# Kernel optimization log

Measured on AMD Instinct MI355X. Metric: run time of the kernel, lower is better.

Reference implementation:

```python
import jax, jax.numpy as jnp
import numpy as np

B, T, DM, DS = 8, 2048, 1024, 256
BASE_DECAY = 0.05


def _lin(k, out_dim, in_dim):
    return jax.random.normal(k, (out_dim, in_dim), jnp.float32) / np.sqrt(in_dim).astype(np.float32)


def setup_inputs() -> dict:
    key = jax.random.key(0)
    ks = jax.random.split(key, 18)
    return {
        "x": jax.random.normal(ks[0], (B, T, DM), jnp.float32),
        "prev_state": jax.random.normal(ks[1], (B, DS), jnp.float32),
        "W_in": _lin(ks[2], DS, DM),
        "W_x": _lin(ks[3], DS, DM),
        "W_s": _lin(ks[4], DS, DS),
        "W_out": _lin(ks[5], DM, DS),
        "W_gx": _lin(ks[6], DS, DM),
        "b_gx": jax.random.normal(ks[7], (DS,), jnp.float32) * 0.02,
        "W_gs": _lin(ks[8], DS, DS),
        "b_gs": jax.random.normal(ks[9], (DS,), jnp.float32) * 0.02,
        "W_dc": _lin(ks[10], DS, DM + DS),
        "b_dc": jax.random.normal(ks[11], (DS,), jnp.float32) * 0.02,
        "W_pp": _lin(ks[12], DS, 2 * DS),
        "b_pp": jax.random.normal(ks[13], (DS,), jnp.float32) * 0.02,
        "W_pg": _lin(ks[14], DS, DS),
        "b_pg": jax.random.normal(ks[15], (DS,), jnp.float32) * 0.02,
    }


def reference(x, prev_state, W_in, W_x, W_s, W_out, W_gx, b_gx, W_gs, b_gs,
              W_dc, b_dc, W_pp, b_pp, W_pg, b_pg):
    # torch Linear: y = x @ W.T (+ b); W is [out, in]
    lin = lambda v, W: jnp.einsum('bti,oi->bto', v, W)
    Bx, Tx, _ = x.shape
    delta = lin(x, W_in)                                   # [B,T,DS]
    s_prev = jnp.broadcast_to(prev_state[:, None, :], (Bx, Tx, prev_state.shape[-1]))
    ctx = jnp.concatenate([x, s_prev], axis=-1)            # [B,T,DM+DS]
    decay = jnp.exp(-BASE_DECAY * jnp.clip(jax.nn.sigmoid(lin(ctx, W_dc) + b_dc), 0.0, 1.0))
    s_pred = s_prev * decay + delta + lin(x, W_x) + 0.5 * lin(s_prev, W_s)
    perturb_in = jnp.concatenate([s_pred, s_prev], axis=-1)  # [B,T,2*DS]
    perturb_vec = jnp.tanh(lin(perturb_in, W_pp) + b_pp)
    perturb_strength = jax.nn.sigmoid(lin(s_prev, W_pg) + b_pg)
    s_corrected = s_pred + perturb_strength * perturb_vec
    gate_in = jax.nn.sigmoid(lin(x, W_gx) + b_gx)
    gate_state = jax.nn.sigmoid(lin(s_prev, W_gs) + b_gs)
    h = s_corrected * gate_in * gate_state
    out = lin(h, W_out)                                    # [B,T,DM]
    return out, h[:, -1, :]
```

## Files before the change

kernel.cpp:

```cpp
#include <hip/hip_runtime.h>
#include <hip/hip_bf16.h>
#include <math.h>


typedef __attribute__((ext_vector_type(4)))  float f32x4;
typedef __attribute__((ext_vector_type(8)))  short bf16x8;

#define DEV static __device__ __forceinline__

DEV float bf2f(short u) {
  union { float f; unsigned i; } v; v.i = ((unsigned)(unsigned short)u) << 16; return v.f;
}
DEV short f2bf(float f) {
  union { float f; unsigned i; } v; v.f = f;
  unsigned x = v.i;
  return (short)((x + 0x7fffu + ((x >> 16) & 1u)) >> 16);
}
DEV unsigned pk_bf16(float lo, float hi) {
  __hip_bfloat162 h = __float22bfloat162_rn(make_float2(lo, hi));
  return *(unsigned*)&h;
}
DEV float sigmoidf_(float x) { return 1.f / (1.f + expf(-x)); }

DEV void gl16(const void* g, void* l) {
  __builtin_amdgcn_global_load_lds(
      (const __attribute__((address_space(1))) void*)(g),
      (__attribute__((address_space(3))) void*)(l), 16, 0, 0);
}

static const size_t OFF_S    = 0;
static const size_t OFF_G    = 8388608;
static const size_t OFF_XBF  = 25165824;
static const size_t OFF_WCAT = OFF_XBF + 33554432;
static const size_t OFF_WPP  = OFF_WCAT + 1572864;
static const size_t OFF_WOUT = OFF_WPP + 131072;
static const size_t OFF_VEC  = OFF_WOUT + 524288;

__global__ __launch_bounds__(256, 1) void prep_all_k(
    const float* __restrict__ x, short* __restrict__ xbf,
    const float* __restrict__ W_in, const float* __restrict__ W_x,
    const float* __restrict__ W_gx, const float* __restrict__ W_dc,
    const float* __restrict__ W_pp, const float* __restrict__ W_out,
    short* __restrict__ wcat, short* __restrict__ wpp, short* __restrict__ wout,
    const float* __restrict__ prev, const float* __restrict__ Ws,
    const float* __restrict__ bdc, const float* __restrict__ bpp,
    const float* __restrict__ Wpg, const float* __restrict__ bpg,
    const float* __restrict__ Wgs, const float* __restrict__ bgs,
    float* __restrict__ vecs) {
  const int bid = (int)blockIdx.x, tid = (int)threadIdx.x;
  if (bid < 8192) {
    const size_t i = ((size_t)bid * 256 + tid) * 8;
    const float4 a = *(const float4*)(x + i);
    const float4 b = *(const float4*)(x + i + 4);
    uint4 o;
    o.x = pk_bf16(a.x, a.y); o.y = pk_bf16(a.z, a.w);
    o.z = pk_bf16(b.x, b.y); o.w = pk_bf16(b.z, b.w);
    *(uint4*)(xbf + i) = o;
  } else if (bid < 12544) {
    const int idx = (bid - 8192) * 256 + tid;
    const int N_WCAT = 768 * 1024, N_WPP = 256 * 256;
    if (idx < N_WCAT) {
      const int r = idx >> 10, k = idx & 1023;
      const int g = r / 192, j = r % 192;
      float v;
      if (j < 64)       v = W_in[(g * 64 + j) * 1024 + k] + W_x[(g * 64 + j) * 1024 + k];
      else if (j < 128) v = W_gx[(g * 64 + j - 64) * 1024 + k];
      else              v = W_dc[(g * 64 + j - 128) * 1280 + k];
      wcat[idx] = f2bf(v);
    } else if (idx < N_WCAT + N_WPP) {
      const int j = idx - N_WCAT, o = j >> 8, k = j & 255;
      wpp[j] = f2bf(W_pp[o * 512 + k]);
    } else {
      const int j = idx - N_WCAT - N_WPP, o = j >> 8, k = j & 255;
      wout[j] = f2bf(W_out[o * 256 + k]);
    }
  } else {
    const int sb = bid - 12544;
    const int b = sb / 20, rem = sb % 20, m = rem >> 2, oq = rem & 3;
    const int lane = tid & 63, w = tid >> 6;
    const float4 sv = *(const float4*)(prev + b * 256 + lane * 4);
    const float* Wb; const float* bias; int stride, off;
    if (m == 0)      { Wb = W_dc; stride = 1280; off = 1024; bias = bdc; }
    else if (m == 1) { Wb = Ws;   stride = 256;  off = 0;    bias = nullptr; }
    else if (m == 2) { Wb = W_pp; stride = 512;  off = 256;  bias = bpp; }
    else if (m == 3) { Wb = Wpg;  stride = 256;  off = 0;    bias = bpg; }
    else             { Wb = Wgs;  stride = 256;  off = 0;    bias = bgs; }
    const int o0 = oq * 64 + w * 16;
#pragma unroll 4
    for (int i = 0; i < 16; ++i) {
      const int o = o0 + i;
      const float4 wv = *(const float4*)(Wb + (size_t)o * stride + off + lane * 4);
      float p = wv.x * sv.x + wv.y * sv.y + wv.z * sv.z + wv.w * sv.w;
#pragma unroll
      for (int d = 32; d >= 1; d >>= 1) p += __shfl_xor(p, d, 64);
      if (lane == 0) {
        float r = (m == 1) ? 0.5f * p : p + bias[o];
        if (m >= 3) r = sigmoidf_(r);
        vecs[m * 2048 + b * 256 + o] = r;
      }
    }
  }
}

__global__ __launch_bounds__(512) void gemm1sg8p_k(const short* __restrict__ A,
                                                   const short* __restrict__ Bm,
                                                   const float* __restrict__ prev,
                                                   const float* __restrict__ bgx,
                                                   const float* __restrict__ vecs,
                                                   short* __restrict__ S,
                                                   short* __restrict__ G) {
  __shared__ short As[4][8192];
  __shared__ short Bs[2][12288];
  const int tid = (int)threadIdx.x, lane = tid & 63, w = tid >> 6;
  int bid = (int)blockIdx.x;
  bid = (bid & 7) * 32 + (bid >> 3);
  const int mt = bid >> 2, grp = bid & 3;
  const int m0 = mt * 256, b = m0 >> 11;
  const short* gA = A + (size_t)m0 * 1024;
  const short* gB = Bm + (size_t)(grp * 192) * 1024;

  f32x4 acc[2][12];
#pragma unroll
  for (int mi = 0; mi < 2; ++mi)
#pragma unroll
    for (int ni = 0; ni < 12; ++ni)
#pragma unroll
      for (int r = 0; r < 4; ++r) acc[mi][ni][r] = 0.f;

#define STGA(lds, half, t)                                                    \
  {                                                                           \
    _Pragma("unroll")                                                         \
    for (int j = 0; j < 2; ++j) {                                             \
      const int Gr = j * 512 + tid, r = Gr >> 3, g = Gr & 7;                  \
      gl16(gA + (size_t)((half) * 128 + r) * 1024 + (t) * 64 +                \
               ((g ^ (r & 7)) * 8),                                           \
           (lds) + Gr * 8);                                                   \
    }                                                                         \
  }
#define STGB(lds, t)                                                          \
  {                                                                           \
    _Pragma("unroll")                                                         \
    for (int j = 0; j < 3; ++j) {                                             \
      const int Gr = j * 512 + tid, r = Gr >> 3, g = Gr & 7;                  \
      gl16(gB + (size_t)r * 1024 + (t) * 64 + ((g ^ (r & 7)) * 8),            \
           (lds) + Gr * 8);                                                   \
    }                                                                         \
  }

  STGA(As[0], 0, 0); STGA(As[1], 1, 0);
  STGB(Bs[0], 0);
  STGA(As[2], 0, 1);
  asm volatile("s_waitcnt vmcnt(2)" ::: "memory");
  __builtin_amdgcn_s_barrier();

  const int arow = lane & 15, ag = lane >> 4;
  const int rA = (w & 3) * 32;
  const int hA = w >> 2;
  bf16x8 af[2][2], bfv[4][2];
#pragma unroll 1
  for (int t = 0; t < 16; ++t) {
    const short* sA = As[(2 * t + hA) & 3];
    const short* sB = Bs[t & 1];
#pragma unroll
    for (int q = 0; q < 3; ++q) {
      if (q == 0) {
#pragma unroll
        for (int mi = 0; mi < 2; ++mi) {
          const int r = rA + mi * 16 + arow;
#pragma unroll
          for (int ks = 0; ks < 2; ++ks)
            af[mi][ks] = *(const bf16x8*)(sA + r * 64 + (((ks * 4 + ag) ^ (r & 7)) << 3));
        }
      }
#pragma unroll
      for (int fj = 0; fj < 4; ++fj) {
        const int r = q * 64 + fj * 16 + arow;
#pragma unroll
        for (int ks = 0; ks < 2; ++ks)
          bfv[fj][ks] = *(const bf16x8*)(sB + r * 64 + (((ks * 4 + ag) ^ (r & 7)) << 3));
      }
      if (q == 0) {
        if (t + 1 < 16) {
          STGB(Bs[(t + 1) & 1], t + 1);
          STGA(As[(2 * t + 3) & 3], 1, t + 1);
        }
      } else if (q == 2) {
        if (t + 2 < 16) STGA(As[(2 * t + 4) & 3], 0, t + 2);
        if (t <= 13) { asm volatile("s_waitcnt vmcnt(2)" ::: "memory"); }
        else         { asm volatile("s_waitcnt vmcnt(0)" ::: "memory"); }
      }
      __builtin_amdgcn_s_barrier();
      __builtin_amdgcn_s_setprio(1);
#pragma unroll
      for (int mi = 0; mi < 2; ++mi)
#pragma unroll
        for (int fj = 0; fj < 4; ++fj)
#pragma unroll
          for (int ks = 0; ks < 2; ++ks)
            acc[mi][q * 4 + fj] = __builtin_amdgcn_mfma_f32_16x16x32_bf16(
                af[mi][ks], bfv[fj][ks], acc[mi][q * 4 + fj], 0, 0, 0);
      __builtin_amdgcn_s_setprio(0);
      __builtin_amdgcn_s_barrier();
    }
  }
#undef STGA
#undef STGB

  const int quad = lane >> 4;
#pragma unroll
  for (int cidx = 0; cidx < 4; ++cidx) {
    const int cg = grp * 64 + cidx * 16 + arow;
    const float sdc = vecs[0 * 2048 + b * 256 + cg];
    const float sws = vecs[1 * 2048 + b * 256 + cg];
    const float pv  = prev[b * 256 + cg];
    const float bg  = bgx[cg];
#pragma unroll
    for (int mi = 0; mi < 2; ++mi)
#pragma unroll
      for (int r = 0; r < 4; ++r) {
        const int row = m0 + w * 32 + mi * 16 + quad * 4 + r;
        const float dec = expf(-0.05f * sigmoidf_(acc[mi][8 + cidx][r] + sdc));
        const float sp = pv * dec + acc[mi][cidx][r] + sws;
        const float g = sigmoidf_(acc[mi][4 + cidx][r] + bg);
        S[(size_t)row * 256 + cg] = f2bf(sp);
        G[(size_t)row * 256 + cg] = f2bf(g);
      }
  }
}

__global__ __launch_bounds__(256) void gemm2h_k(const short* __restrict__ S,
                                                const short* __restrict__ G,
                                                const short* __restrict__ Wpp,
                                                const float* __restrict__ vecs,
                                                short* __restrict__ H,
                                                float* __restrict__ out) {
  __shared__ short As2[2][2048];
  __shared__ short Bs2[2][4096];
  const int tid = (int)threadIdx.x, lane = tid & 63, w = tid >> 6;
  const int wr = w >> 1, wc = w & 1;
  int bid = (int)blockIdx.x;
  bid = (bid & 7) * 64 + (bid >> 3);
  const int m0 = (bid >> 1) * 64, n0 = (bid & 1) * 128;
  const int b = m0 >> 11;
  const short* gA = S + (size_t)m0 * 256;
  const short* gB = Wpp + (size_t)n0 * 256;

  f32x4 acc[2][4];
#pragma unroll
  for (int mi = 0; mi < 2; ++mi)
#pragma unroll
    for (int ni = 0; ni < 4; ++ni)
#pragma unroll
      for (int r = 0; r < 4; ++r) acc[mi][ni][r] = 0.f;

#define STAGE2(buf, t)                                                        \
  {                                                                           \
    {                                                                         \
      const int g = tid;                                                      \
      gl16(gA + (size_t)(g >> 2) * 256 + (t) * 32 + (g & 3) * 8,              \
           As2[buf] + w * 512);                                               \
    }                                                                         \
    _Pragma("unroll")                                                         \
    for (int j = 0; j < 2; ++j) {                                             \
      const int g = j * 256 + tid;                                            \
      gl16(gB + (size_t)(g >> 2) * 256 + (t) * 32 + (g & 3) * 8,              \
           Bs2[buf] + (j * 256 + w * 64) * 8);                                \
    }                                                                         \
  }

  STAGE2(0, 0);
  __syncthreads();
  const int arow = lane & 15, ag = lane >> 4;
#pragma unroll 1
  for (int t = 0; t < 8; ++t) {
    if (t < 7) STAGE2((t + 1) & 1, t + 1);
    const short* Asb = As2[t & 1];
    const short* Bsb = Bs2[t & 1];
    bf16x8 af[2], bfv[4];
#pragma unroll
    for (int mi = 0; mi < 2; ++mi)
      af[mi] = *(const bf16x8*)(Asb + (wr * 32 + mi * 16 + arow) * 32 + ag * 8);
#pragma unroll
    for (int ni = 0; ni < 4; ++ni)
      bfv[ni] = *(const bf16x8*)(Bsb + (wc * 64 + ni * 16 + arow) * 32 + ag * 8);
#pragma unroll
    for (int mi = 0; mi < 2; ++mi)
#pragma unroll
      for (int ni = 0; ni < 4; ++ni)
        acc[mi][ni] = __builtin_amdgcn_mfma_f32_16x16x32_bf16(af[mi], bfv[ni], acc[mi][ni], 0, 0, 0);
    __syncthreads();
  }
#undef STAGE2

#pragma unroll
  for (int mi = 0; mi < 2; ++mi)
#pragma unroll
    for (int ni = 0; ni < 4; ++ni) {
      const int col = n0 + wc * 64 + ni * 16 + (lane & 15);
      const float spp  = vecs[2 * 2048 + b * 256 + col];
      const float pstr = vecs[3 * 2048 + b * 256 + col];
      const float gst  = vecs[4 * 2048 + b * 256 + col];
#pragma unroll
      for (int r = 0; r < 4; ++r) {
        const int row = m0 + wr * 32 + mi * 16 + (lane >> 4) * 4 + r;
        const float pv = tanhf(acc[mi][ni][r] + spp);
        const float sp = bf2f(S[(size_t)row * 256 + col]);
        const float h = (sp + pstr * pv) * bf2f(G[(size_t)row * 256 + col]) * gst;
        H[(size_t)row * 256 + col] = f2bf(h);
        if ((row & 2047) == 2047) out[16777216 + b * 256 + col] = h;
      }
    }
}

__global__ __launch_bounds__(256) void gemm3_k(const short* __restrict__ H,
                                               const short* __restrict__ Wout,
                                               float* __restrict__ out) {
  __shared__ short As3[2][2048];
  __shared__ short Bs3[2][8192];
  const int tid = (int)threadIdx.x, lane = tid & 63, w = tid >> 6;
  const int wr = w >> 1, wc = w & 1;
  int bid = (int)blockIdx.x;
  bid = (bid & 7) * 128 + (bid >> 3);
  const int m0 = (bid >> 2) * 64, n0 = (bid & 3) * 256;
  const short* gA = H + (size_t)m0 * 256;
  const short* gB = Wout + (size_t)n0 * 256;

  f32x4 acc[2][8];
#pragma unroll
  for (int mi = 0; mi < 2; ++mi)
#pragma unroll
    for (int ni = 0; ni < 8; ++ni)
#pragma unroll
      for (int r = 0; r < 4; ++r) acc[mi][ni][r] = 0.f;

#define STAGE3(buf, t)                                                        \
  {                                                                           \
    {                                                                         \
      const int g = tid;                                                      \
      gl16(gA + (size_t)(g >> 2) * 256 + (t) * 32 + (g & 3) * 8,              \
           As3[buf] + w * 512);                                               \
    }                                                                         \
    _Pragma("unroll")                                                         \
    for (int j = 0; j < 4; ++j) {                                             \
      const int g = j * 256 + tid;                                            \
      gl16(gB + (size_t)(g >> 2) * 256 + (t) * 32 + (g & 3) * 8,              \
           Bs3[buf] + (j * 256 + w * 64) * 8);                                \
    }                                                                         \
  }

  STAGE3(0, 0);
  __syncthreads();
  const int arow = lane & 15, ag = lane >> 4;
#pragma unroll 1
  for (int t = 0; t < 8; ++t) {
    if (t < 7) STAGE3((t + 1) & 1, t + 1);
    const short* Asb = As3[t & 1];
    const short* Bsb = Bs3[t & 1];
    bf16x8 af[2], bfv[8];
#pragma unroll
    for (int mi = 0; mi < 2; ++mi)
      af[mi] = *(const bf16x8*)(Asb + (wr * 32 + mi * 16 + arow) * 32 + ag * 8);
#pragma unroll
    for (int ni = 0; ni < 8; ++ni)
      bfv[ni] = *(const bf16x8*)(Bsb + (wc * 128 + ni * 16 + arow) * 32 + ag * 8);
#pragma unroll
    for (int mi = 0; mi < 2; ++mi)
#pragma unroll
      for (int ni = 0; ni < 8; ++ni)
        acc[mi][ni] = __builtin_amdgcn_mfma_f32_16x16x32_bf16(af[mi], bfv[ni], acc[mi][ni], 0, 0, 0);
    __syncthreads();
  }
#undef STAGE3

#pragma unroll
  for (int mi = 0; mi < 2; ++mi)
#pragma unroll
    for (int ni = 0; ni < 8; ++ni) {
      const int col = n0 + wc * 128 + ni * 16 + (lane & 15);
#pragma unroll
      for (int r = 0; r < 4; ++r) {
        const int row = m0 + wr * 32 + mi * 16 + (lane >> 4) * 4 + r;
        out[(size_t)row * 1024 + col] = acc[mi][ni][r];
      }
    }
}

extern "C" void kernel_launch(void* const* d_in, const int* in_sizes, int n_in,
                              void* d_out, int out_size, void* d_ws, size_t ws_size,
                              hipStream_t stream) {
  (void)in_sizes; (void)n_in; (void)out_size; (void)ws_size;
  const float* x      = (const float*)d_in[0];
  const float* prev   = (const float*)d_in[1];
  const float* W_in   = (const float*)d_in[2];
  const float* W_x    = (const float*)d_in[3];
  const float* W_s    = (const float*)d_in[4];
  const float* W_out  = (const float*)d_in[5];
  const float* W_gx   = (const float*)d_in[6];
  const float* b_gx   = (const float*)d_in[7];
  const float* W_gs   = (const float*)d_in[8];
  const float* b_gs   = (const float*)d_in[9];
  const float* W_dc   = (const float*)d_in[10];
  const float* b_dc   = (const float*)d_in[11];
  const float* W_pp   = (const float*)d_in[12];
  const float* b_pp   = (const float*)d_in[13];
  const float* W_pg   = (const float*)d_in[14];
  const float* b_pg   = (const float*)d_in[15];

  char* ws = (char*)d_ws;
  short* S    = (short*)(ws + OFF_S);
  short* G    = (short*)(ws + OFF_G);
  short* xbf  = (short*)(ws + OFF_XBF);
  short* H    = (short*)(ws + OFF_XBF);
  short* wcat = (short*)(ws + OFF_WCAT);
  short* wpp  = (short*)(ws + OFF_WPP);
  short* wout = (short*)(ws + OFF_WOUT);
  float* vecs = (float*)(ws + OFF_VEC);
  float* out  = (float*)d_out;

  prep_all_k<<<12704, 256, 0, stream>>>(x, xbf, W_in, W_x, W_gx, W_dc, W_pp, W_out,
                                        wcat, wpp, wout, prev, W_s, b_dc, b_pp,
                                        W_pg, b_pg, W_gs, b_gs, vecs);
  gemm1sg8p_k<<<256, 512, 0, stream>>>(xbf, wcat, prev, b_gx, vecs, S, G);
  gemm2h_k<<<512, 256, 0, stream>>>(S, G, wpp, vecs, H, out);
  gemm3_k<<<1024, 256, 0, stream>>>(H, wout, out);
}
```

Before: 104.7 us.

## Shrink gemm1 M-tile to 128 rows with simpler double-buffered pipeline

The first fused GEMM drops from 256-row to 128-row M tiles, so the grid doubles from 256 to 512 blocks, and each wave now owns one 16-row A fragment instead of two. The staggered 4-buffer A / 2-buffer B schedule, with per-quarter barriers and partial waitcnt, is replaced by a plain double buffer: issue the next tile's loads, compute the current tile with interleaved LDS reads and MFMAs, then wait for all loads and barrier. This should improve occupancy and load balance across CUs and lower register pressure. The cost is half the reuse of each B tile, so global and LDS traffic for B doubles, and the full vmcnt(0) wait leaves less room to overlap loads with compute.

```diff
diff --git a/kernel.cpp b/kernel.cpp
--- a/kernel.cpp
+++ b/kernel.cpp
@@ -102,106 +102,81 @@
   }
 }
 
-__global__ __launch_bounds__(512) void gemm1sg8p_k(const short* __restrict__ A,
-                                                   const short* __restrict__ Bm,
-                                                   const float* __restrict__ prev,
-                                                   const float* __restrict__ bgx,
-                                                   const float* __restrict__ vecs,
-                                                   short* __restrict__ S,
-                                                   short* __restrict__ G) {
-  __shared__ short As[4][8192];
+__global__ __launch_bounds__(512) void gemm1sg_k(const short* __restrict__ A,
+                                                 const short* __restrict__ Bm,
+                                                 const float* __restrict__ prev,
+                                                 const float* __restrict__ bgx,
+                                                 const float* __restrict__ vecs,
+                                                 short* __restrict__ S,
+                                                 short* __restrict__ G) {
+  __shared__ short As[2][8192];
   __shared__ short Bs[2][12288];
   const int tid = (int)threadIdx.x, lane = tid & 63, w = tid >> 6;
   int bid = (int)blockIdx.x;
-  bid = (bid & 7) * 32 + (bid >> 3);
+  bid = (bid & 7) * 64 + (bid >> 3);
   const int mt = bid >> 2, grp = bid & 3;
-  const int m0 = mt * 256, b = m0 >> 11;
+  const int m0 = mt * 128, b = m0 >> 11;
   const short* gA = A + (size_t)m0 * 1024;
   const short* gB = Bm + (size_t)(grp * 192) * 1024;
 
-  f32x4 acc[2][12];
-#pragma unroll
-  for (int mi = 0; mi < 2; ++mi)
-#pragma unroll
-    for (int ni = 0; ni < 12; ++ni)
-#pragma unroll
-      for (int r = 0; r < 4; ++r) acc[mi][ni][r] = 0.f;
-
-#define STGA(lds, half, t)                                                    \
+  f32x4 acc[12];
+#pragma unroll
+  for (int ni = 0; ni < 12; ++ni)
+#pragma unroll
+    for (int r = 0; r < 4; ++r) acc[ni][r] = 0.f;
+
+#define STGA(buf, t)                                                          \
   {                                                                           \
     _Pragma("unroll")                                                         \
     for (int j = 0; j < 2; ++j) {                                             \
       const int Gr = j * 512 + tid, r = Gr >> 3, g = Gr & 7;                  \
-      gl16(gA + (size_t)((half) * 128 + r) * 1024 + (t) * 64 +                \
-               ((g ^ (r & 7)) * 8),                                           \
-           (lds) + Gr * 8);                                                   \
-    }                                                                         \
-  }
-#define STGB(lds, t)                                                          \
+      gl16(gA + (size_t)r * 1024 + (t) * 64 + ((g ^ (r & 7)) * 8),            \
+           As[buf] + Gr * 8);                                                 \
+    }                                                                         \
+  }
+#define STGB(buf, t)                                                          \
   {                                                                           \
     _Pragma("unroll")                                                         \
     for (int j = 0; j < 3; ++j) {                                             \
       const int Gr = j * 512 + tid, r = Gr >> 3, g = Gr & 7;                  \
       gl16(gB + (size_t)r * 1024 + (t) * 64 + ((g ^ (r & 7)) * 8),            \
-           (lds) + Gr * 8);                                                   \
-    }                                                                         \
-  }
-
-  STGA(As[0], 0, 0); STGA(As[1], 1, 0);
-  STGB(Bs[0], 0);
-  STGA(As[2], 0, 1);
-  asm volatile("s_waitcnt vmcnt(2)" ::: "memory");
+           Bs[buf] + Gr * 8);                                                 \
+    }                                                                         \
+  }
+
+  STGA(0, 0); STGB(0, 0);
+  asm volatile("s_waitcnt vmcnt(0)" ::: "memory");
   __builtin_amdgcn_s_barrier();
 
   const int arow = lane & 15, ag = lane >> 4;
-  const int rA = (w & 3) * 32;
-  const int hA = w >> 2;
-  bf16x8 af[2][2], bfv[4][2];
+  const int rowA = w * 16 + arow;
+  const int swzA = rowA & 7;
 #pragma unroll 1
   for (int t = 0; t < 16; ++t) {
-    const short* sA = As[(2 * t + hA) & 3];
+    const short* sA = As[t & 1];
     const short* sB = Bs[t & 1];
+    if (t < 15) { STGA((t + 1) & 1, t + 1); STGB((t + 1) & 1, t + 1); }
+    bf16x8 af[2];
+#pragma unroll
+    for (int ks = 0; ks < 2; ++ks)
+      af[ks] = *(const bf16x8*)(sA + rowA * 64 + (((ks * 4 + ag) ^ swzA) << 3));
+    __builtin_amdgcn_s_setprio(1);
 #pragma unroll
     for (int q = 0; q < 3; ++q) {
-      if (q == 0) {
-#pragma unroll
-        for (int mi = 0; mi < 2; ++mi) {
-          const int r = rA + mi * 16 + arow;
-#pragma unroll
-          for (int ks = 0; ks < 2; ++ks)
-            af[mi][ks] = *(const bf16x8*)(sA + r * 64 + (((ks * 4 + ag) ^ (r & 7)) << 3));
+#pragma unroll
+      for (int fj = 0; fj < 4; ++fj) {
+        const int r = q * 64 + fj * 16 + arow;
+#pragma unroll
+        for (int ks = 0; ks < 2; ++ks) {
+          const bf16x8 bf = *(const bf16x8*)(sB + r * 64 + (((ks * 4 + ag) ^ (r & 7)) << 3));
+          acc[q * 4 + fj] = __builtin_amdgcn_mfma_f32_16x16x32_bf16(
+              af[ks], bf, acc[q * 4 + fj], 0, 0, 0);
         }
       }
-#pragma unroll
-      for (int fj = 0; fj < 4; ++fj) {
-        const int r = q * 64 + fj * 16 + arow;
-#pragma unroll
-        for (int ks = 0; ks < 2; ++ks)
-          bfv[fj][ks] = *(const bf16x8*)(sB + r * 64 + (((ks * 4 + ag) ^ (r & 7)) << 3));
-      }
-      if (q == 0) {
-        if (t + 1 < 16) {
-          STGB(Bs[(t + 1) & 1], t + 1);
-          STGA(As[(2 * t + 3) & 3], 1, t + 1);
-        }
-      } else if (q == 2) {
-        if (t + 2 < 16) STGA(As[(2 * t + 4) & 3], 0, t + 2);
-        if (t <= 13) { asm volatile("s_waitcnt vmcnt(2)" ::: "memory"); }
-        else         { asm volatile("s_waitcnt vmcnt(0)" ::: "memory"); }
-      }
-      __builtin_amdgcn_s_barrier();
-      __builtin_amdgcn_s_setprio(1);
-#pragma unroll
-      for (int mi = 0; mi < 2; ++mi)
-#pragma unroll
-        for (int fj = 0; fj < 4; ++fj)
-#pragma unroll
-          for (int ks = 0; ks < 2; ++ks)
-            acc[mi][q * 4 + fj] = __builtin_amdgcn_mfma_f32_16x16x32_bf16(
-                af[mi][ks], bfv[fj][ks], acc[mi][q * 4 + fj], 0, 0, 0);
-      __builtin_amdgcn_s_setprio(0);
-      __builtin_amdgcn_s_barrier();
-    }
+    }
+    __builtin_amdgcn_s_setprio(0);
+    if (t < 15) { asm volatile("s_waitcnt vmcnt(0)" ::: "memory"); }
+    __builtin_amdgcn_s_barrier();
   }
 #undef STGA
 #undef STGB
@@ -215,16 +190,14 @@
     const float pv  = prev[b * 256 + cg];
     const float bg  = bgx[cg];
 #pragma unroll
-    for (int mi = 0; mi < 2; ++mi)
-#pragma unroll
-      for (int r = 0; r < 4; ++r) {
-        const int row = m0 + w * 32 + mi * 16 + quad * 4 + r;
-        const float dec = expf(-0.05f * sigmoidf_(acc[mi][8 + cidx][r] + sdc));
-        const float sp = pv * dec + acc[mi][cidx][r] + sws;
-        const float g = sigmoidf_(acc[mi][4 + cidx][r] + bg);
-        S[(size_t)row * 256 + cg] = f2bf(sp);
-        G[(size_t)row * 256 + cg] = f2bf(g);
-      }
+    for (int r = 0; r < 4; ++r) {
+      const int row = m0 + w * 16 + quad * 4 + r;
+      const float dec = expf(-0.05f * sigmoidf_(acc[8 + cidx][r] + sdc));
+      const float sp = pv * dec + acc[cidx][r] + sws;
+      const float g = sigmoidf_(acc[4 + cidx][r] + bg);
+      S[(size_t)row * 256 + cg] = f2bf(sp);
+      G[(size_t)row * 256 + cg] = f2bf(g);
+    }
   }
 }
 
@@ -420,7 +393,7 @@
   prep_all_k<<<12704, 256, 0, stream>>>(x, xbf, W_in, W_x, W_gx, W_dc, W_pp, W_out,
                                         wcat, wpp, wout, prev, W_s, b_dc, b_pp,
                                         W_pg, b_pg, W_gs, b_gs, vecs);
-  gemm1sg8p_k<<<256, 512, 0, stream>>>(xbf, wcat, prev, b_gx, vecs, S, G);
+  gemm1sg_k<<<512, 512, 0, stream>>>(xbf, wcat, prev, b_gx, vecs, S, G);
   gemm2h_k<<<512, 256, 0, stream>>>(S, G, wpp, vecs, H, out);
   gemm3_k<<<1024, 256, 0, stream>>>(H, wout, out);
 }
```

Result: faster. 100.4 us (-4.1%).
